# Performance work log

Measured on AMD Instinct MI355X. Metric: run time of the kernel, lower is better.

Reference implementation:

```python
import jax, jax.numpy as jnp
import numpy as np

C = 256; Ca = C // 2; WH = 8; WW = 8; K = 3; NH = 8; HD = Ca // NH
EPS_LN = 1e-5; EPS_BN = 1e-5

def _rel_pos_idx(wh, ww):
    coords = np.stack(np.meshgrid(np.arange(wh), np.arange(ww), indexing='ij'))  # (2,wh,ww)
    flat = coords.reshape(2, -1)
    rel = (flat[:, :, None] - flat[:, None, :]).transpose(1, 2, 0).astype(np.int64)  # (N,N,2)
    rel[..., 0] += wh - 1
    rel[..., 1] += ww - 1
    rel[..., 0] *= 2 * ww - 1
    return jnp.asarray(rel.sum(-1))  # (N,N)

REL_IDX = _rel_pos_idx(WH, WW)

def _ln(x, g, b):
    m = x.mean(-1, keepdims=True)
    v = x.var(-1, keepdims=True)
    return (x - m) / jnp.sqrt(v + EPS_LN) * g + b

def _bn(x, g, b):  # eval-mode BN, running_mean=0, running_var=1; x is NCHW
    return x * (g / np.sqrt(1.0 + EPS_BN))[None, :, None, None] + b[None, :, None, None]

def _conv1x1(x, w, b):  # w: (O, I)
    return jnp.einsum('bchw,oc->bohw', x, w) + b[None, :, None, None]

def _rwp(x, h, w, wh, ww):  # windows (B*nW, wh*ww, c) -> image (B, c, h, w)
    Bn, N, c = x.shape
    nh, nw = h // wh, w // ww
    B = Bn // (nh * nw)
    x = x.reshape(B, nh, nw, wh, ww, c)
    return x.transpose(0, 5, 1, 3, 2, 4).reshape(B, c, h, w)

def _wp(x, wh, ww):  # image (B, c, h, w) -> windows (B*nW, wh*ww, c)
    B, c, h, w = x.shape
    x = x.reshape(B, c, h // wh, wh, w // ww, ww)
    return x.transpose(0, 2, 4, 3, 5, 1).reshape(-1, wh * ww, c)

def _gelu(t):
    return jax.nn.gelu(t, approximate=False)

def forward(x, rel_pos_bias, attn_w, attn_b, attn_ln_g, attn_ln_b,
            conv_w, conv_b, conv_bn_g, conv_bn_b,
            ci_w1, ci_b1, ci_bn_g, ci_bn_b, ci_w2, ci_b2,
            pr_w, pr_b, cn_bn_g, cn_bn_b,
            qkv_w, qkv_b,
            si_w1, si_b1, si_bn_g, si_bn_b, si_w2, si_b2,
            an_g, an_b, out_w, out_b, h, w):
    B_, N, Cfull = x.shape
    x_attn = _ln(x @ attn_w + attn_b, attn_ln_g, attn_ln_b)  # (B_, N, Ca)
    # conv branch -- note: source applies RWP to raw x (proj_cnn output is dead code)
    x_img = _rwp(x, h, w, WH, WW)  # (B, C, h, w)
    pad = K // 2
    x_cnn = jax.lax.conv_general_dilated(
        x_img, conv_w, (1, 1), [(pad, pad), (pad, pad)],
        dimension_numbers=('NCHW', 'OIHW', 'NCHW'), feature_group_count=Cfull)
    x_cnn = _gelu(_bn(x_cnn + conv_b[None, :, None, None], conv_bn_g, conv_bn_b))
    gap = x_cnn.mean((2, 3), keepdims=True)  # (B, C, 1, 1)
    ci = _conv1x1(gap, ci_w1, ci_b1)
    ci = _gelu(_bn(ci, ci_bn_g, ci_bn_b))
    ci = _conv1x1(ci, ci_w2, ci_b2)  # (B, Ca, 1, 1)
    x_cnn = _conv1x1(x_cnn, pr_w, pr_b)  # (B, Ca, h, w)
    # windowed attention
    qkv = (x_attn @ qkv_w + qkv_b).reshape(B_, N, 3, NH, HD).transpose(2, 0, 3, 1, 4)
    q, k, v = qkv[0], qkv[1], qkv[2]  # each (B_, NH, N, HD)
    B = ci.shape[0]
    ci_s = jax.nn.sigmoid(ci).reshape(B, 1, NH, 1, HD)
    v = (v.reshape(B, B_ // B, NH, N, HD) * ci_s).reshape(B_, NH, N, HD)
    scale = HD ** -0.5
    attn = jnp.einsum('bhnd,bhmd->bhnm', q * scale, k)
    bias = rel_pos_bias[REL_IDX]  # (N, N, NH)
    attn = jax.nn.softmax(attn + bias.transpose(2, 0, 1)[None], axis=-1)
    x_attn = jnp.einsum('bhnm,bhmd->bhnd', attn, v).transpose(0, 2, 1, 3).reshape(B_, N, Ca)
    # spatial interaction gating of conv branch
    x_sp = _rwp(x_attn, h, w, WH, WW)  # (B, Ca, h, w)
    si = _conv1x1(x_sp, si_w1, si_b1)
    si = _gelu(_bn(si, si_bn_g, si_bn_b))
    si = _conv1x1(si, si_w2, si_b2)  # (B, 1, h, w)
    x_cnn = jax.nn.sigmoid(si * x_cnn)
    x_cnn = _bn(x_cnn, cn_bn_g, cn_bn_b)
    x_cnn = _wp(x_cnn, WH, WW)  # (B_, N, Ca)
    x_attn = _ln(x_attn, an_g, an_b)
    return jnp.concatenate([x_attn, x_cnn], axis=-1) @ out_w + out_b

def setup_inputs() -> dict:
    key = jax.random.key(0)
    ks = jax.random.split(key, 12)
    B_, N = 2048, WH * WW
    s = 0.02
    return dict(
        x=jax.random.normal(ks[0], (B_, N, C), jnp.float32),
        rel_pos_bias=jax.random.uniform(ks[1], ((2 * WH - 1) * (2 * WW - 1), NH), jnp.float32),
        attn_w=jax.random.normal(ks[2], (C, Ca)) * s, attn_b=jnp.zeros((Ca,)),
        attn_ln_g=jnp.ones((Ca,)), attn_ln_b=jnp.zeros((Ca,)),
        conv_w=jax.random.normal(ks[3], (C, 1, K, K)) * s, conv_b=jnp.zeros((C,)),
        conv_bn_g=jnp.ones((C,)), conv_bn_b=jnp.zeros((C,)),
        ci_w1=jax.random.normal(ks[4], (C // 8, C)) * s, ci_b1=jnp.zeros((C // 8,)),
        ci_bn_g=jnp.ones((C // 8,)), ci_bn_b=jnp.zeros((C // 8,)),
        ci_w2=jax.random.normal(ks[5], (Ca, C // 8)) * s, ci_b2=jnp.zeros((Ca,)),
        pr_w=jax.random.normal(ks[6], (Ca, C)) * s, pr_b=jnp.zeros((Ca,)),
        cn_bn_g=jnp.ones((Ca,)), cn_bn_b=jnp.zeros((Ca,)),
        qkv_w=jax.random.normal(ks[7], (Ca, 3 * Ca)) * s, qkv_b=jnp.zeros((3 * Ca,)),
        si_w1=jax.random.normal(ks[8], (C // 16, Ca)) * s, si_b1=jnp.zeros((C // 16,)),
        si_bn_g=jnp.ones((C // 16,)), si_bn_b=jnp.zeros((C // 16,)),
        si_w2=jax.random.normal(ks[9], (1, C // 16)) * s, si_b2=jnp.zeros((1,)),
        an_g=jnp.ones((Ca,)), an_b=jnp.zeros((Ca,)),
        out_w=jax.random.normal(ks[10], (C, C)) * s, out_b=jnp.zeros((C,)),
        h=64, w=64,
    )

def reference(x, rel_pos_bias, attn_w, attn_b, attn_ln_g, attn_ln_b,
              conv_w, conv_b, conv_bn_g, conv_bn_b,
              ci_w1, ci_b1, ci_bn_g, ci_bn_b, ci_w2, ci_b2,
              pr_w, pr_b, cn_bn_g, cn_bn_b,
              qkv_w, qkv_b,
              si_w1, si_b1, si_bn_g, si_bn_b, si_w2, si_b2,
              an_g, an_b, out_w, out_b, h, w):
    return forward(x, rel_pos_bias, attn_w, attn_b, attn_ln_g, attn_ln_b,
                   conv_w, conv_b, conv_bn_g, conv_bn_b,
                   ci_w1, ci_b1, ci_bn_g, ci_bn_b, ci_w2, ci_b2,
                   pr_w, pr_b, cn_bn_g, cn_bn_b,
                   qkv_w, qkv_b,
                   si_w1, si_b1, si_bn_g, si_bn_b, si_w2, si_b2,
                   an_g, an_b, out_w, out_b, h, w)
```

## Files before the change

### kernel.cpp

```cpp
#include <hip/hip_runtime.h>
#include <math.h>


#define BNR 0.9999950000374998f

typedef __attribute__((ext_vector_type(8))) short short8;
typedef __attribute__((ext_vector_type(4))) float f32x4;
typedef __attribute__((ext_vector_type(4))) _Float16 half4;
typedef __attribute__((ext_vector_type(8))) _Float16 half8;
typedef __attribute__((ext_vector_type(2))) _Float16 h2v;

__device__ __forceinline__ float gelu_f(float x) {
  const float z = x * (1.0f + 0.044715f * x * x);
  return x / (1.0f + __expf(-1.5957691216057308f * z));
}
__device__ __forceinline__ unsigned short f2bf(float f) {
  unsigned int u = __builtin_bit_cast(unsigned int, f);
  u += 0x7fffu + ((u >> 16) & 1u);
  return (unsigned short)(u >> 16);
}
__device__ __forceinline__ float bf2f(unsigned short h) {
  unsigned int u = ((unsigned int)h) << 16;
  return __builtin_bit_cast(float, u);
}
__device__ __forceinline__ void ld8(const unsigned short* p, float* o) {
  const short8 v = *(const short8*)p;
#pragma unroll
  for (int i = 0; i < 8; ++i) o[i] = bf2f((unsigned short)v[i]);
}
__device__ __forceinline__ unsigned int pkh(float a, float b) {
  return __builtin_bit_cast(unsigned int, __builtin_amdgcn_cvt_pkrtz(a, b));
}

#define ATI(r, ch) (((r) << 8) + ((((ch) ^ ((r)&7))) << 3))

__global__ __launch_bounds__(256) void kpack(
    const float* __restrict__ aw, const float* __restrict__ qw,
    const float* __restrict__ prw, const float* __restrict__ ow,
    const float* __restrict__ sw1, unsigned short* __restrict__ awp,
    unsigned short* __restrict__ qwp, unsigned short* __restrict__ prwp,
    unsigned short* __restrict__ owp, unsigned short* __restrict__ sw1p) {
  const int b = blockIdx.x;
  const float* src; unsigned short* dst; int fs, K, N, NT, trans, f16o;
  if (b < 64)       { fs = b;       src = aw;  dst = awp;  K = 256; N = 128; NT = 8;  trans = 0; f16o = 0; }
  else if (b < 160) { fs = b - 64;  src = qw;  dst = qwp;  K = 128; N = 384; NT = 24; trans = 0; f16o = 0; }
  else if (b < 224) { fs = b - 160; src = prw; dst = prwp; K = 256; N = 128; NT = 8;  trans = 1; f16o = 1; }
  else if (b < 352) { fs = b - 224; src = ow;  dst = owp;  K = 256; N = 256; NT = 16; trans = 0; f16o = 0; }
  else              { fs = b - 352; src = sw1; dst = sw1p; K = 128; N = 16;  NT = 1;  trans = 1; f16o = 0; }
  const int ks = fs / NT, nt = fs % NT;
  for (int idx = threadIdx.x; idx < 512; idx += 256) {
    const int l = idx >> 3, i = idx & 7;
    const int k = ks * 32 + ((l >> 4) << 3) + i, n = nt * 16 + (l & 15);
    const float v = trans ? src[n * K + k] : src[k * N + n];
    dst[(fs * 64 + l) * 8 + i] =
        f16o ? __builtin_bit_cast(unsigned short, (_Float16)v) : f2bf(v);
  }
}

__global__ __launch_bounds__(256) void kbias(const float* __restrict__ rpb,
                                             unsigned short* __restrict__ bt) {
  const int i = blockIdx.x * 256 + threadIdx.x;
  const int h = i >> 12, n = (i >> 6) & 63, m = i & 63;
  const int ny = n >> 3, nx = n & 7, my = m >> 3, mx = m & 7;
  const float v = rpb[((ny - my + 7) * 15 + (nx - mx + 7)) * 8 + h];
  bt[i] = __builtin_bit_cast(unsigned short, (_Float16)v);
}

__global__ __launch_bounds__(256) void k1_attn_ln(
    const float* __restrict__ x, const unsigned short* __restrict__ awp,
    const float* __restrict__ ab, const float* __restrict__ lg,
    const float* __restrict__ lb, unsigned short* __restrict__ xattn,
    unsigned short* __restrict__ xb) {
  const int tid = threadIdx.x, w = tid >> 6, l = tid & 63;
  const int lr = l & 15, lg4 = l >> 4;
  const int r0 = blockIdx.x * 64 + w * 16;
  const float* xp = x + (size_t)(r0 + lr) * 256 + lg4 * 8;
  unsigned short* xbp = xb + (size_t)(r0 + lr) * 256 + lg4 * 8;
  short8 a[8];
#pragma unroll
  for (int ks = 0; ks < 8; ++ks) {
    const float4 f0 = *(const float4*)(xp + ks * 32);
    const float4 f1 = *(const float4*)(xp + ks * 32 + 4);
    short8 av;
    av[0] = f2bf(f0.x); av[1] = f2bf(f0.y); av[2] = f2bf(f0.z); av[3] = f2bf(f0.w);
    av[4] = f2bf(f1.x); av[5] = f2bf(f1.y); av[6] = f2bf(f1.z); av[7] = f2bf(f1.w);
    a[ks] = av;
    uint4 hv;
    hv.x = pkh(f0.x, f0.y); hv.y = pkh(f0.z, f0.w);
    hv.z = pkh(f1.x, f1.y); hv.w = pkh(f1.z, f1.w);
    *(uint4*)(xbp + ks * 32) = hv;
  }
  f32x4 acc[8];
#pragma unroll
  for (int nt = 0; nt < 8; ++nt) acc[nt] = (f32x4)0.f;
#pragma unroll
  for (int nt = 0; nt < 8; ++nt)
#pragma unroll
    for (int ks = 0; ks < 8; ++ks) {
      const short8 bfr = *(const short8*)(awp + ((ks * 8 + nt) * 64 + l) * 8);
      acc[nt] = __builtin_amdgcn_mfma_f32_16x16x32_bf16(a[ks], bfr, acc[nt], 0, 0, 0);
    }
  float bias[8], gam[8], bet[8];
#pragma unroll
  for (int nt = 0; nt < 8; ++nt) {
    const int col = nt * 16 + lr;
    bias[nt] = ab[col]; gam[nt] = lg[col]; bet[nt] = lb[col];
  }
#pragma unroll
  for (int j = 0; j < 4; ++j) {
    float s = 0.f, qq = 0.f;
#pragma unroll
    for (int nt = 0; nt < 8; ++nt) {
      const float v = acc[nt][j] + bias[nt];
      acc[nt][j] = v; s += v; qq += v * v;
    }
    s += __shfl_xor(s, 1); s += __shfl_xor(s, 2);
    s += __shfl_xor(s, 4); s += __shfl_xor(s, 8);
    qq += __shfl_xor(qq, 1); qq += __shfl_xor(qq, 2);
    qq += __shfl_xor(qq, 4); qq += __shfl_xor(qq, 8);
    const float mean = s * (1.f / 128.f);
    const float var = qq * (1.f / 128.f) - mean * mean;
    const float rstd = rsqrtf(var + 1e-5f);
    const int row = r0 + lg4 * 4 + j;
#pragma unroll
    for (int nt = 0; nt < 8; ++nt)
      xattn[(size_t)row * 128 + nt * 16 + lr] =
          f2bf((acc[nt][j] - mean) * rstd * gam[nt] + bet[nt]);
  }
}

__global__ __launch_bounds__(256) void k25_conv(
    const unsigned short* __restrict__ xb, const float* __restrict__ cw,
    const float* __restrict__ cb, const float* __restrict__ bg,
    const float* __restrict__ bb, const unsigned short* __restrict__ prwp,
    const float* __restrict__ prb, unsigned short* __restrict__ xpr,
    float* __restrict__ gpart) {
  __shared__ unsigned short gl[32][264];
  const int tid = threadIdx.x;
  const int bid = (blockIdx.x & 7) * 512 + (blockIdx.x >> 3);
  const int b = bid >> 7;
  const int y = (bid >> 1) & 63;
  const int xt = (bid & 1) * 32;
  const int w = tid >> 6, l = tid & 63;
  {
    const int c0 = l << 2;
    h2v w01[9], w23[9];
#pragma unroll
    for (int k = 0; k < 9; ++k) {
      w01[k][0] = (_Float16)cw[(c0 + 0) * 9 + k];
      w01[k][1] = (_Float16)cw[(c0 + 1) * 9 + k];
      w23[k][0] = (_Float16)cw[(c0 + 2) * 9 + k];
      w23[k][1] = (_Float16)cw[(c0 + 3) * 9 + k];
    }
    const float4 cbf = *(const float4*)&cb[c0];
    float4 scf = *(const float4*)&bg[c0];
    scf.x *= BNR; scf.y *= BNR; scf.z *= BNR; scf.w *= BNR;
    const float4 sbf = *(const float4*)&bb[c0];
    h2v cb01 = {(_Float16)cbf.x, (_Float16)cbf.y};
    h2v cb23 = {(_Float16)cbf.z, (_Float16)cbf.w};
    h2v sc01 = {(_Float16)scf.x, (_Float16)scf.y};
    h2v sc23 = {(_Float16)scf.z, (_Float16)scf.w};
    h2v sb01 = {(_Float16)sbf.x, (_Float16)sbf.y};
    h2v sb23 = {(_Float16)sbf.z, (_Float16)sbf.w};
    float4 gsum = make_float4(0.f, 0.f, 0.f, 0.f);
    const int px0 = xt + w * 8;
#pragma unroll
    for (int sc2 = 0; sc2 < 2; ++sc2) {
      const int p0 = px0 + sc2 * 4;
      h2v v0[3][6], v1[3][6];
#pragma unroll
      for (int dy = 0; dy < 3; ++dy) {
        const int yy = y + dy - 1;
        const bool vy = (unsigned)yy < 64u;
        const int ybase = vy ? ((b * 64 + (yy >> 3) * 8) * 64 + (yy & 7) * 8) : 0;
#pragma unroll
        for (int q = 0; q < 6; ++q) {
          const int xx = p0 - 1 + q;
          h2v a = (h2v)(_Float16)0.f, c = (h2v)(_Float16)0.f;
          if (vy && (unsigned)xx < 64u) {
            const int row = ybase + (xx >> 3) * 64 + (xx & 7);
            const uint2 u = *(const uint2*)&xb[(size_t)row * 256 + c0];
            a = __builtin_bit_cast(h2v, u.x);
            c = __builtin_bit_cast(h2v, u.y);
          }
          v0[dy][q] = a; v1[dy][q] = c;
        }
      }
#pragma unroll
      for (int p = 0; p < 4; ++p) {
        h2v s0 = cb01, s1 = cb23;
#pragma unroll
        for (int dy = 0; dy < 3; ++dy)
#pragma unroll
          for (int dx = 0; dx < 3; ++dx) {
            s0 = w01[dy * 3 + dx] * v0[dy][p + dx] + s0;
            s1 = w23[dy * 3 + dx] * v1[dy][p + dx] + s1;
          }
        s0 = s0 * sc01 + sb01;
        s1 = s1 * sc23 + sb23;
        const float g0 = gelu_f((float)s0[0]), g1 = gelu_f((float)s0[1]);
        const float g2 = gelu_f((float)s1[0]), g3 = gelu_f((float)s1[1]);
        uint2 pk;
        pk.x = pkh(g0, g1); pk.y = pkh(g2, g3);
        *(uint2*)&gl[w * 8 + sc2 * 4 + p][c0] = pk;
        gsum.x += g0; gsum.y += g1; gsum.z += g2; gsum.w += g3;
      }
    }
    *(float4*)&gpart[(size_t)bid * 256 + c0] = gsum;
  }
  __syncthreads();
  const int lr = l & 15, lg4 = l >> 4;
  const int mr0 = (w & 1) * 16, nt0 = (w >> 1) * 4;
  half8 a[8];
#pragma unroll
  for (int ks = 0; ks < 8; ++ks)
    a[ks] = __builtin_bit_cast(half8,
                               *(const short8*)&gl[mr0 + lr][ks * 32 + lg4 * 8]);
  f32x4 acc[4];
#pragma unroll
  for (int nt = 0; nt < 4; ++nt) acc[nt] = (f32x4)0.f;
#pragma unroll
  for (int nt = 0; nt < 4; ++nt)
#pragma unroll
    for (int ks = 0; ks < 8; ++ks) {
      const half8 bfr = __builtin_bit_cast(
          half8, *(const short8*)(prwp + ((ks * 8 + nt0 + nt) * 64 + l) * 8));
      acc[nt] = __builtin_amdgcn_mfma_f32_16x16x32_f16(a[ks], bfr, acc[nt], 0, 0, 0);
    }
#pragma unroll
  for (int nt = 0; nt < 4; ++nt) {
    const int col = (nt0 + nt) * 16 + lr;
    const float bv = prb[col];
#pragma unroll
    for (int j = 0; j < 4; ++j) {
      const int pix = (b * 64 + y) * 64 + xt + mr0 + lg4 * 4 + j;
      xpr[(size_t)pix * 128 + col] = f2bf(acc[nt][j] + bv);
    }
  }
}

__global__ __launch_bounds__(128) void k3_ci(
    const float* __restrict__ gp, const float* __restrict__ w1,
    const float* __restrict__ b1, const float* __restrict__ g1,
    const float* __restrict__ bb1, const float* __restrict__ w2,
    const float* __restrict__ b2, float* __restrict__ cis) {
  __shared__ float gm[256];
  __shared__ float c1[32];
  const int b = blockIdx.x, tid = threadIdx.x;
  for (int c = tid; c < 256; c += 128) {
    float s = 0.f;
    for (int p = 0; p < 128; ++p) s += gp[(size_t)(b * 128 + p) * 256 + c];
    gm[c] = s * (1.f / 4096.f);
  }
  __syncthreads();
  if (tid < 32) {
    float s = b1[tid];
    for (int c = 0; c < 256; ++c) s = fmaf(gm[c], w1[tid * 256 + c], s);
    s = s * (g1[tid] * BNR) + bb1[tid];
    c1[tid] = gelu_f(s);
  }
  __syncthreads();
  float s = b2[tid];
#pragma unroll
  for (int i = 0; i < 32; ++i) s = fmaf(c1[i], w2[tid * 32 + i], s);
  cis[b * 128 + tid] = 1.f / (1.f + __expf(-s));
}

__global__ __launch_bounds__(256, 4) void k4_attn(
    const unsigned short* __restrict__ xa, const unsigned short* __restrict__ qwp,
    const float* __restrict__ qb, const float* __restrict__ cis,
    const unsigned short* __restrict__ biasT, unsigned short* __restrict__ attn) {
  __shared__ _Float16 QS[4][64][38];
  __shared__ _Float16 KS[4][64][38];
  const int tid = threadIdx.x;
  const int win = blockIdx.x, img = win >> 6;
  const int w = tid >> 6, l = tid & 63, lr = l & 15, lg4 = l >> 4;
  {
    float qbv[4];
#pragma unroll
    for (int t = 0; t < 4; ++t) {
      const int gnt = (t < 2) ? (2 * w + t) : (8 + 2 * w + t - 2);
      qbv[t] = qb[gnt * 16 + lr];
    }
    f32x4 acc[4][4];
#pragma unroll
    for (int mt = 0; mt < 4; ++mt)
#pragma unroll
      for (int t = 0; t < 4; ++t) acc[mt][t] = (f32x4)0.f;
#pragma unroll
    for (int ks = 0; ks < 4; ++ks) {
      short8 a[4];
#pragma unroll
      for (int mt = 0; mt < 4; ++mt)
        a[mt] = *(const short8*)(xa + (size_t)(win * 64 + mt * 16 + lr) * 128 +
                                 ks * 32 + lg4 * 8);
#pragma unroll
      for (int t = 0; t < 4; ++t) {
        const int gnt = (t < 2) ? (2 * w + t) : (8 + 2 * w + t - 2);
        const short8 bfr = *(const short8*)(qwp + ((ks * 24 + gnt) * 64 + l) * 8);
#pragma unroll
        for (int mt = 0; mt < 4; ++mt)
          acc[mt][t] = __builtin_amdgcn_mfma_f32_16x16x32_bf16(a[mt], bfr,
                                                               acc[mt][t], 0, 0, 0);
      }
    }
#pragma unroll
    for (int mt = 0; mt < 4; ++mt)
#pragma unroll
      for (int t = 0; t < 4; ++t)
#pragma unroll
        for (int j = 0; j < 4; ++j) {
          const int row = mt * 16 + lg4 * 4 + j;
          const float v = acc[mt][t][j] + qbv[t];
          if (t < 2) QS[w][row][t * 16 + lr] = (_Float16)(v * 0.25f);
          else KS[w][row][(t - 2) * 16 + lr] = (_Float16)v;
        }
  }
  half4 bV2[2][4];
  {
    float qbv[2], cisv[2];
#pragma unroll
    for (int t = 0; t < 2; ++t) {
      qbv[t] = qb[(16 + 2 * w + t) * 16 + lr];
      cisv[t] = cis[img * 128 + (2 * w + t) * 16 + lr];
    }
    f32x4 accv[4][2];
#pragma unroll
    for (int mt = 0; mt < 4; ++mt)
#pragma unroll
      for (int t = 0; t < 2; ++t) accv[mt][t] = (f32x4)0.f;
#pragma unroll
    for (int ks = 0; ks < 4; ++ks) {
      short8 a[4];
#pragma unroll
      for (int mt = 0; mt < 4; ++mt)
        a[mt] = *(const short8*)(xa + (size_t)(win * 64 + mt * 16 + lr) * 128 +
                                 ks * 32 + lg4 * 8);
#pragma unroll
      for (int t = 0; t < 2; ++t) {
        const short8 bfr =
            *(const short8*)(qwp + ((ks * 24 + 16 + 2 * w + t) * 64 + l) * 8);
#pragma unroll
        for (int mt = 0; mt < 4; ++mt)
          accv[mt][t] = __builtin_amdgcn_mfma_f32_16x16x32_bf16(a[mt], bfr,
                                                                accv[mt][t], 0, 0, 0);
      }
    }
#pragma unroll
    for (int t = 0; t < 2; ++t)
#pragma unroll
      for (int kt = 0; kt < 4; ++kt) {
        half4 p;
#pragma unroll
        for (int i = 0; i < 4; ++i)
          p[i] = (_Float16)((accv[kt][t][i] + qbv[t]) * cisv[t]);
        bV2[t][kt] = p;
      }
  }
  for (int hi = 0; hi < 2; ++hi) {
    const int h = w * 2 + hi;
    half4 aK[4], bQ[4];
#pragma unroll
    for (int mt = 0; mt < 4; ++mt)
      aK[mt] = *(const half4*)&KS[w][mt * 16 + lr][hi * 16 + lg4 * 4];
#pragma unroll
    for (int nt = 0; nt < 4; ++nt)
      bQ[nt] = *(const half4*)&QS[w][nt * 16 + lr][hi * 16 + lg4 * 4];
    f32x4 s[4][4];
#pragma unroll
    for (int mt = 0; mt < 4; ++mt)
#pragma unroll
      for (int nt = 0; nt < 4; ++nt)
        s[mt][nt] = __builtin_amdgcn_mfma_f32_16x16x16f16(aK[mt], bQ[nt],
                                                          (f32x4)0.f, 0, 0, 0);
#pragma unroll
    for (int nt = 0; nt < 4; ++nt) {
      const int n = nt * 16 + lr;
      const unsigned short* bp = biasT + (((h << 6) + n) << 6);
#pragma unroll
      for (int mt = 0; mt < 4; ++mt) {
        const half4 b4 = *(const half4*)(bp + mt * 16 + lg4 * 4);
        s[mt][nt][0] += (float)b4[0];
        s[mt][nt][1] += (float)b4[1];
        s[mt][nt][2] += (float)b4[2];
        s[mt][nt][3] += (float)b4[3];
      }
    }
    float inv[4];
#pragma unroll
    for (int nt = 0; nt < 4; ++nt) {
      float m0 = -1e30f;
#pragma unroll
      for (int mt = 0; mt < 4; ++mt)
#pragma unroll
        for (int r = 0; r < 4; ++r) m0 = fmaxf(m0, s[mt][nt][r]);
      m0 = fmaxf(m0, __shfl_xor(m0, 16));
      m0 = fmaxf(m0, __shfl_xor(m0, 32));
      float d0 = 0.f;
#pragma unroll
      for (int mt = 0; mt < 4; ++mt)
#pragma unroll
        for (int r = 0; r < 4; ++r) {
          const float e = __expf(s[mt][nt][r] - m0);
          s[mt][nt][r] = e;
          d0 += e;
        }
      d0 += __shfl_xor(d0, 16);
      d0 += __shfl_xor(d0, 32);
      inv[nt] = 1.f / d0;
    }
    half4 pa[4][4];
#pragma unroll
    for (int nt = 0; nt < 4; ++nt)
#pragma unroll
      for (int kt = 0; kt < 4; ++kt) {
        half4 p;
#pragma unroll
        for (int r = 0; r < 4; ++r) p[r] = (_Float16)(s[kt][nt][r] * inv[nt]);
        pa[nt][kt] = p;
      }
    f32x4 o[4];
#pragma unroll
    for (int nt = 0; nt < 4; ++nt) o[nt] = (f32x4)0.f;
#pragma unroll
    for (int nt = 0; nt < 4; ++nt)
#pragma unroll
      for (int kt = 0; kt < 4; ++kt)
        o[nt] = __builtin_amdgcn_mfma_f32_16x16x16f16(pa[nt][kt], bV2[hi][kt],
                                                      o[nt], 0, 0, 0);
#pragma unroll
    for (int nt = 0; nt < 4; ++nt)
#pragma unroll
      for (int r = 0; r < 4; ++r) {
        const int token = win * 64 + nt * 16 + lg4 * 4 + r;
        attn[(size_t)token * 128 + h * 16 + lr] = f2bf(o[nt][r]);
      }
  }
}

__global__ __launch_bounds__(256) void k6_tail(
    const unsigned short* __restrict__ attn, const unsigned short* __restrict__ xpr,
    const unsigned short* __restrict__ sw1p, const float* __restrict__ sb1,
    const float* __restrict__ sgc, const float* __restrict__ sbc,
    const float* __restrict__ sw2, const float* __restrict__ sb2,
    const float* __restrict__ cg, const float* __restrict__ cbb,
    const float* __restrict__ ag, const float* __restrict__ abb,
    const unsigned short* __restrict__ owp, const float* __restrict__ ob,
    float* __restrict__ out) {
  __shared__ unsigned short At[64 * 256];
  __shared__ float sifl[64];
  __shared__ float statl[64][2];
  const int tid = threadIdx.x;
  const int R0 = blockIdx.x * 64;
  const int w = tid >> 6, l = tid & 63, lr = l & 15, lg4 = l >> 4;
  for (int i = tid; i < 1024; i += 256) {
    const int r = i >> 4, c16 = i & 15;
    *(uint4*)&At[ATI(r, c16)] =
        *(const uint4*)&attn[(size_t)(R0 + r) * 128 + c16 * 8];
    const int R = R0 + r, win = R >> 6, tt = R & 63;
    const int bimg = win >> 6, wy = (win >> 3) & 7, wx = win & 7;
    const int pix = (bimg * 64 + wy * 8 + (tt >> 3)) * 64 + wx * 8 + (tt & 7);
    *(uint4*)&At[ATI(r, 16 + c16)] =
        *(const uint4*)&xpr[(size_t)pix * 128 + c16 * 8];
  }
  __syncthreads();
  {
    const int r = tid >> 2, q = tid & 3;
    float xv[32];
#pragma unroll
    for (int b8 = 0; b8 < 4; ++b8) ld8(&At[ATI(r, q * 4 + b8)], xv + b8 * 8);
    float ps = 0.f, pq = 0.f;
#pragma unroll
    for (int j = 0; j < 32; ++j) { ps += xv[j]; pq += xv[j] * xv[j]; }
    ps += __shfl_xor(ps, 1); ps += __shfl_xor(ps, 2);
    pq += __shfl_xor(pq, 1); pq += __shfl_xor(pq, 2);
    if (q == 0) {
      const float mean = ps * (1.f / 128.f);
      const float var = pq * (1.f / 128.f) - mean * mean;
      statl[r][0] = mean;
      statl[r][1] = rsqrtf(var + 1e-5f);
    }
  }
  {
    const int row = w * 16 + lr;
    f32x4 sa = (f32x4)0.f;
#pragma unroll
    for (int ks = 0; ks < 4; ++ks) {
      const short8 a4 = *(const short8*)&At[ATI(row, ks * 4 + lg4)];
      const short8 bfr = *(const short8*)(sw1p + (ks * 64 + l) * 8);
      sa = __builtin_amdgcn_mfma_f32_16x16x32_bf16(a4, bfr, sa, 0, 0, 0);
    }
    const float sb1v = sb1[lr], g1v = sgc[lr] * BNR, b1v = sbc[lr];
    const float w2v = sw2[lr], sb2v = sb2[0];
#pragma unroll
    for (int j = 0; j < 4; ++j) {
      float s = (sa[j] + sb1v) * g1v + b1v;
      float p = gelu_f(s) * w2v;
      p += __shfl_xor(p, 1); p += __shfl_xor(p, 2);
      p += __shfl_xor(p, 4); p += __shfl_xor(p, 8);
      if (lr == 0) sifl[w * 16 + lg4 * 4 + j] = p + sb2v;
    }
  }
  __syncthreads();
  {
    const int c = tid & 127;
    const float agv = ag[c], abbv = abb[c];
    const float cgv = cg[c] * BNR, cbbv = cbb[c];
#pragma unroll
    for (int k = 0; k < 32; ++k) {
      const int r = (tid >> 7) + k * 2;
      const int ia = ATI(r, c >> 3) + (c & 7);
      const int ic = ATI(r, 16 + (c >> 3)) + (c & 7);
      float a = bf2f(At[ia]);
      a = (a - statl[r][0]) * statl[r][1] * agv + abbv;
      At[ia] = f2bf(a);
      const float cv = bf2f(At[ic]);
      const float g = 1.f / (1.f + __expf(-sifl[r] * cv));
      At[ic] = f2bf(g * cgv + cbbv);
    }
  }
  __syncthreads();
  const int row = w * 16 + lr;
  short8 a[8];
#pragma unroll
  for (int ks = 0; ks < 8; ++ks)
    a[ks] = *(const short8*)&At[ATI(row, ks * 4 + lg4)];
  f32x4 acc[16];
#pragma unroll
  for (int nt = 0; nt < 16; ++nt) acc[nt] = (f32x4)0.f;
#pragma unroll
  for (int nt = 0; nt < 16; ++nt)
#pragma unroll
    for (int ks = 0; ks < 8; ++ks) {
      const short8 bfr = *(const short8*)(owp + ((ks * 16 + nt) * 64 + l) * 8);
      acc[nt] = __builtin_amdgcn_mfma_f32_16x16x32_bf16(a[ks], bfr, acc[nt], 0, 0, 0);
    }
#pragma unroll
  for (int nt = 0; nt < 16; ++nt) {
    const int col = nt * 16 + lr;
    const float bv = ob[col];
#pragma unroll
    for (int j = 0; j < 4; ++j)
      out[(size_t)(R0 + w * 16 + lg4 * 4 + j) * 256 + col] = acc[nt][j] + bv;
  }
}

extern "C" void kernel_launch(void* const* d_in, const int* in_sizes, int n_in,
                              void* d_out, int out_size, void* d_ws,
                              size_t ws_size, hipStream_t stream) {
  (void)in_sizes; (void)n_in; (void)out_size; (void)ws_size;
  const float* x      = (const float*)d_in[0];
  const float* rpb    = (const float*)d_in[1];
  const float* attn_w = (const float*)d_in[2];
  const float* attn_b = (const float*)d_in[3];
  const float* aln_g  = (const float*)d_in[4];
  const float* aln_b  = (const float*)d_in[5];
  const float* conv_w = (const float*)d_in[6];
  const float* conv_b = (const float*)d_in[7];
  const float* cbn_g  = (const float*)d_in[8];
  const float* cbn_b  = (const float*)d_in[9];
  const float* ci_w1  = (const float*)d_in[10];
  const float* ci_b1  = (const float*)d_in[11];
  const float* ci_bg  = (const float*)d_in[12];
  const float* ci_bb  = (const float*)d_in[13];
  const float* ci_w2  = (const float*)d_in[14];
  const float* ci_b2  = (const float*)d_in[15];
  const float* pr_w   = (const float*)d_in[16];
  const float* pr_b   = (const float*)d_in[17];
  const float* cn_g   = (const float*)d_in[18];
  const float* cn_b   = (const float*)d_in[19];
  const float* qkv_w  = (const float*)d_in[20];
  const float* qkv_b  = (const float*)d_in[21];
  const float* si_w1  = (const float*)d_in[22];
  const float* si_b1  = (const float*)d_in[23];
  const float* si_bg  = (const float*)d_in[24];
  const float* si_bb  = (const float*)d_in[25];
  const float* si_w2  = (const float*)d_in[26];
  const float* si_b2  = (const float*)d_in[27];
  const float* an_g   = (const float*)d_in[28];
  const float* an_b   = (const float*)d_in[29];
  const float* out_w  = (const float*)d_in[30];
  const float* out_b  = (const float*)d_in[31];

  unsigned short* xb    = (unsigned short*)d_ws;
  unsigned short* xattn = xb + 33554432;
  unsigned short* attn  = xattn + 16777216;
  unsigned short* xpr   = attn + 16777216;
  float* gpart = (float*)(xpr + 16777216);
  float* cis   = gpart + 1048576;
  unsigned short* awp   = (unsigned short*)(cis + 4096);
  unsigned short* qwp   = awp + 32768;
  unsigned short* prwp  = qwp + 49152;
  unsigned short* owp   = prwp + 32768;
  unsigned short* sw1p  = owp + 65536;
  unsigned short* biasT = sw1p + 2048;

  kpack<<<356, 256, 0, stream>>>(attn_w, qkv_w, pr_w, out_w, si_w1,
                                 awp, qwp, prwp, owp, sw1p);
  kbias<<<128, 256, 0, stream>>>(rpb, biasT);
  k1_attn_ln<<<2048, 256, 0, stream>>>(x, awp, attn_b, aln_g, aln_b, xattn, xb);
  k25_conv<<<4096, 256, 0, stream>>>(xb, conv_w, conv_b, cbn_g, cbn_b, prwp,
                                     pr_b, xpr, gpart);
  k3_ci<<<32, 128, 0, stream>>>(gpart, ci_w1, ci_b1, ci_bg, ci_bb, ci_w2,
                                ci_b2, cis);
  k4_attn<<<2048, 256, 0, stream>>>(xattn, qwp, qkv_b, cis, biasT, attn);
  k6_tail<<<2048, 256, 0, stream>>>(attn, xpr, sw1p, si_b1, si_bg, si_bb,
                                    si_w2, si_b2, cn_g, cn_b, an_g, an_b,
                                    owp, out_b, (float*)d_out);
}
```

Before: 300.2 us.

## Merge bias-table kernel into pack, stage attention output in LDS for wide stores

The relative-position bias table build moves into the weight-packing kernel as extra blocks, which removes one kernel launch. In the attention kernel, the LDS row padding for Q and K changes, and both heads' Q/K fragments are loaded up front. Each wave's output is then staged in reused Q shared memory and written to global memory as 16-byte vector stores instead of scattered 2-byte stores. This aims to cut launch overhead and improve store coalescing. The cost is possible LDS bank conflicts from the new padding and higher register pressure from holding both heads' fragments.

```diff
diff --git a/kernel.cpp b/kernel.cpp
--- a/kernel.cpp
+++ b/kernel.cpp
@@ -37,10 +37,19 @@
 __global__ __launch_bounds__(256) void kpack(
     const float* __restrict__ aw, const float* __restrict__ qw,
     const float* __restrict__ prw, const float* __restrict__ ow,
-    const float* __restrict__ sw1, unsigned short* __restrict__ awp,
-    unsigned short* __restrict__ qwp, unsigned short* __restrict__ prwp,
-    unsigned short* __restrict__ owp, unsigned short* __restrict__ sw1p) {
+    const float* __restrict__ sw1, const float* __restrict__ rpb,
+    unsigned short* __restrict__ awp, unsigned short* __restrict__ qwp,
+    unsigned short* __restrict__ prwp, unsigned short* __restrict__ owp,
+    unsigned short* __restrict__ sw1p, unsigned short* __restrict__ bt) {
   const int b = blockIdx.x;
+  if (b >= 356) {
+    const int i = (b - 356) * 256 + threadIdx.x;
+    const int h = i >> 12, n = (i >> 6) & 63, m = i & 63;
+    const int ny = n >> 3, nx = n & 7, my = m >> 3, mx = m & 7;
+    const float v = rpb[((ny - my + 7) * 15 + (nx - mx + 7)) * 8 + h];
+    bt[i] = __builtin_bit_cast(unsigned short, (_Float16)v);
+    return;
+  }
   const float* src; unsigned short* dst; int fs, K, N, NT, trans, f16o;
   if (b < 64)       { fs = b;       src = aw;  dst = awp;  K = 256; N = 128; NT = 8;  trans = 0; f16o = 0; }
   else if (b < 160) { fs = b - 64;  src = qw;  dst = qwp;  K = 128; N = 384; NT = 24; trans = 0; f16o = 0; }
@@ -55,15 +64,6 @@
     dst[(fs * 64 + l) * 8 + i] =
         f16o ? __builtin_bit_cast(unsigned short, (_Float16)v) : f2bf(v);
   }
-}
-
-__global__ __launch_bounds__(256) void kbias(const float* __restrict__ rpb,
-                                             unsigned short* __restrict__ bt) {
-  const int i = blockIdx.x * 256 + threadIdx.x;
-  const int h = i >> 12, n = (i >> 6) & 63, m = i & 63;
-  const int ny = n >> 3, nx = n & 7, my = m >> 3, mx = m & 7;
-  const float v = rpb[((ny - my + 7) * 15 + (nx - mx + 7)) * 8 + h];
-  bt[i] = __builtin_bit_cast(unsigned short, (_Float16)v);
 }
 
 __global__ __launch_bounds__(256) void k1_attn_ln(
@@ -270,8 +270,8 @@
     const unsigned short* __restrict__ xa, const unsigned short* __restrict__ qwp,
     const float* __restrict__ qb, const float* __restrict__ cis,
     const unsigned short* __restrict__ biasT, unsigned short* __restrict__ attn) {
-  __shared__ _Float16 QS[4][64][38];
-  __shared__ _Float16 KS[4][64][38];
+  __shared__ _Float16 QS[4][64][36];
+  __shared__ _Float16 KS[4][64][34];
   const int tid = threadIdx.x;
   const int win = blockIdx.x, img = win >> 6;
   const int w = tid >> 6, l = tid & 63, lr = l & 15, lg4 = l >> 4;
@@ -357,15 +357,30 @@
         bV2[t][kt] = p;
       }
   }
+  unsigned short* Ost = (unsigned short*)&QS[w][0][0];
+  half4 aK1[4], bQ1[4];
   for (int hi = 0; hi < 2; ++hi) {
     const int h = w * 2 + hi;
     half4 aK[4], bQ[4];
-#pragma unroll
-    for (int mt = 0; mt < 4; ++mt)
-      aK[mt] = *(const half4*)&KS[w][mt * 16 + lr][hi * 16 + lg4 * 4];
-#pragma unroll
-    for (int nt = 0; nt < 4; ++nt)
-      bQ[nt] = *(const half4*)&QS[w][nt * 16 + lr][hi * 16 + lg4 * 4];
+    if (hi == 0) {
+#pragma unroll
+      for (int mt = 0; mt < 4; ++mt)
+        aK[mt] = *(const half4*)&KS[w][mt * 16 + lr][lg4 * 4];
+#pragma unroll
+      for (int nt = 0; nt < 4; ++nt)
+        bQ[nt] = *(const half4*)&QS[w][nt * 16 + lr][lg4 * 4];
+#pragma unroll
+      for (int mt = 0; mt < 4; ++mt)
+        aK1[mt] = *(const half4*)&KS[w][mt * 16 + lr][16 + lg4 * 4];
+#pragma unroll
+      for (int nt = 0; nt < 4; ++nt)
+        bQ1[nt] = *(const half4*)&QS[w][nt * 16 + lr][16 + lg4 * 4];
+    } else {
+#pragma unroll
+      for (int mt = 0; mt < 4; ++mt) aK[mt] = aK1[mt];
+#pragma unroll
+      for (int nt = 0; nt < 4; ++nt) bQ[nt] = bQ1[nt];
+    }
     f32x4 s[4][4];
 #pragma unroll
     for (int mt = 0; mt < 4; ++mt)
@@ -432,9 +447,19 @@
     for (int nt = 0; nt < 4; ++nt)
 #pragma unroll
       for (int r = 0; r < 4; ++r) {
-        const int token = win * 64 + nt * 16 + lg4 * 4 + r;
-        attn[(size_t)token * 128 + h * 16 + lr] = f2bf(o[nt][r]);
-      }
+        const int token = nt * 16 + lg4 * 4 + r;
+        Ost[token * 36 + hi * 16 + lr] = f2bf(o[nt][r]);
+      }
+  }
+  const int tl = l >> 2, c8 = (l & 3) * 8;
+#pragma unroll
+  for (int it = 0; it < 4; ++it) {
+    const int t = it * 16 + tl;
+    const uint2 lo = *(const uint2*)&Ost[t * 36 + c8];
+    const uint2 hi2 = *(const uint2*)&Ost[t * 36 + c8 + 4];
+    uint4 v;
+    v.x = lo.x; v.y = lo.y; v.z = hi2.x; v.w = hi2.y;
+    *(uint4*)&attn[(size_t)(win * 64 + t) * 128 + w * 32 + c8] = v;
   }
 }
 
@@ -595,9 +620,8 @@
   unsigned short* sw1p  = owp + 65536;
   unsigned short* biasT = sw1p + 2048;
 
-  kpack<<<356, 256, 0, stream>>>(attn_w, qkv_w, pr_w, out_w, si_w1,
-                                 awp, qwp, prwp, owp, sw1p);
-  kbias<<<128, 256, 0, stream>>>(rpb, biasT);
+  kpack<<<484, 256, 0, stream>>>(attn_w, qkv_w, pr_w, out_w, si_w1, rpb,
+                                 awp, qwp, prwp, owp, sw1p, biasT);
   k1_attn_ln<<<2048, 256, 0, stream>>>(x, awp, attn_b, aln_g, aln_b, xattn, xb);
   k25_conv<<<4096, 256, 0, stream>>>(xb, conv_w, conv_b, cbn_g, cbn_b, prwp,
                                      pr_b, xpr, gpart);
```

New measurement: 293.6 us. 1.02x faster.
